# Kernel tuning notes

Hardware: AMD Instinct MI355X
Metric: run time of the kernel (lower is better)

## Reference

```python
import jax, jax.numpy as jnp
import numpy as np

EMB = 256
N_NODES = 100000
N_EDGES = 500000
N_REL = 10
REL_DIM = 64
HID = 128
HEADS = 4
HEAD_DIM = HID // HEADS


def setup_inputs() -> dict:
    key = jax.random.key(0)
    ks = jax.random.split(key, 16)
    s = lambda i, shape: jax.random.normal(ks[i], shape, dtype=jnp.float32) * 0.05
    return {
        "node_embeddings": jax.random.normal(ks[0], (N_NODES, EMB), dtype=jnp.float32),
        "edge_index": jax.random.randint(ks[1], (2, N_EDGES), 0, N_NODES),
        "relation_type": jax.random.randint(ks[2], (N_EDGES,), 0, N_REL),
        "rel_emb": s(3, (N_REL, REL_DIM)),
        "W_edge": s(4, (2 * EMB, HID)), "b_edge": jnp.zeros((HID,), jnp.float32),
        "W_q": s(5, (REL_DIM, HID)), "b_q": jnp.zeros((HID,), jnp.float32),
        "W_k": s(6, (HID, HID)), "b_k": jnp.zeros((HID,), jnp.float32),
        "W_v": s(7, (HID, HID)), "b_v": jnp.zeros((HID,), jnp.float32),
        "W_o1": s(8, (HID, HID)), "b_o1": jnp.zeros((HID,), jnp.float32),
        "W_o2": s(9, (HID, 1)), "b_o2": jnp.zeros((1,), jnp.float32),
    }


def reference(node_embeddings, edge_index, relation_type, rel_emb,
              W_edge, b_edge, W_q, b_q, W_k, b_k, W_v, b_v,
              W_o1, b_o1, W_o2, b_o2):
    # Gather endpoint features: [E, 2*EMB]
    src = node_embeddings[edge_index[0]]
    tgt = node_embeddings[edge_index[1]]
    edge_features = jnp.concatenate([src, tgt], axis=1)
    # Edge MLP (dropout is identity at eval): [E, HID]
    edge_hidden = jax.nn.relu(edge_features @ W_edge + b_edge)
    # Relation embedding lookup: [E, REL_DIM]
    rel = rel_emb[relation_type]
    E = edge_hidden.shape[0]
    Q = (rel @ W_q + b_q).reshape(E, HEADS, HEAD_DIM)
    K = (edge_hidden @ W_k + b_k).reshape(E, HEADS, HEAD_DIM)
    V = (edge_hidden @ W_v + b_v).reshape(E, HEADS, HEAD_DIM)
    scale = jnp.sqrt(jnp.float32(HEAD_DIM))
    scores = jnp.sum(Q * K, axis=-1) / scale          # [E, HEADS]
    attn = jax.nn.softmax(scores, axis=-1)            # softmax over heads
    attended = (attn[..., None] * V).reshape(E, HID)
    output = attended + edge_hidden
    # Output MLP: Linear->ReLU->Linear(1)
    h = jax.nn.relu(output @ W_o1 + b_o1)
    score = (h @ W_o2 + b_o2).squeeze(-1)             # [E]
    return score
```

## Files before the change

kernel.cpp:

```cpp
#include <hip/hip_runtime.h>

#define EMB   256
#define HID   128
#define RELD  64
#define NREL  10
#define TE    64

typedef __attribute__((ext_vector_type(8)))  short bf16x8;
typedef __attribute__((ext_vector_type(16))) float f32x16;

__device__ __forceinline__ float bf16_to_f32(unsigned short u) {
    union { unsigned int i; float f; } v;
    v.i = ((unsigned int)u) << 16;
    return v.f;
}

__device__ __forceinline__ unsigned short f32_to_bf16(float x) {
    union { unsigned int i; float f; } v;
    v.f = x;
    unsigned int b = v.i;
    unsigned int rounded = b + 0x7fffu + ((b >> 16) & 1u);
    return (unsigned short)(rounded >> 16);
}

template <bool F32>
__device__ __forceinline__ float ldx(const void* p, size_t i) {
    if (F32) return ((const float*)p)[i];
    return bf16_to_f32(((const unsigned short*)p)[i]);
}

__device__ __forceinline__ bool detect_f32(const void* nodeEmb) {
    const float* f = (const float*)nodeEmb;
    float x = f[(threadIdx.x & 63) * 997];
    bool sane = isfinite(x) && fabsf(x) < 1.0e6f;
    unsigned long long m = __ballot(sane);
    return __popcll(m) >= 48;
}

template <bool F32>
__device__ void prep_body(int vb, const void* W_edge, const void* W_k,
                          const void* W_v, const void* W_o1, const void* rel_emb,
                          const void* W_q, const void* b_q,
                          unsigned short* WTe, unsigned short* WTk,
                          unsigned short* WTv, unsigned short* WTo1, float* Qtab)
{
    if (vb < 448) {
        int idx = vb * 256 + threadIdx.x;
        if (idx < 65536) {
            int kc = idx >> 12, e = idx & 4095;
            int g = e >> 3, j = e & 7;
            int col = g & 127, kg = g >> 7;
            int k = kc * 32 + kg * 8 + j;
            WTe[idx] = f32_to_bf16(ldx<F32>(W_edge, (size_t)k * HID + col));
        } else if (idx < 65536 + 16384) {
            int i = idx - 65536;
            int kc = i >> 12, e = i & 4095;
            int g = e >> 3, j = e & 7;
            int col = g & 127, kg = (g >> 7) & 3;
            int k = kc * 32 + kg * 8 + j;
            WTk[i] = f32_to_bf16(ldx<F32>(W_k, (size_t)k * HID + col));
        } else if (idx < 65536 + 2 * 16384) {
            int i = idx - 65536 - 16384;
            int kc = i >> 12, e = i & 4095;
            int g = e >> 3, j = e & 7;
            int col = g & 127, kg = (g >> 7) & 3;
            int k = kc * 32 + kg * 8 + j;
            WTv[i] = f32_to_bf16(ldx<F32>(W_v, (size_t)k * HID + col));
        } else {
            int i = idx - 65536 - 2 * 16384;
            int kc = i >> 12, e = i & 4095;
            int g = e >> 3, j = e & 7;
            int col = g & 127, kg = (g >> 7) & 3;
            int k = kc * 32 + kg * 8 + j;
            WTo1[i] = f32_to_bf16(ldx<F32>(W_o1, (size_t)k * HID + col));
        }
    } else {
        const int t = threadIdx.x;
        const int c = t & (HID - 1);
        const int h = t >> 7;
        for (int r = h; r < NREL; r += 2) {
            float acc = 0.f;
            for (int d = 0; d < RELD; ++d)
                acc += ldx<F32>(rel_emb, r * RELD + d) * ldx<F32>(W_q, (size_t)d * HID + c);
            Qtab[r * HID + c] = acc + ldx<F32>(b_q, c);
        }
    }
}

__global__ void prep_kernel(const void* nodeEmb,
                            const void* W_edge, const void* W_k, const void* W_v,
                            const void* W_o1, const void* rel_emb, const void* W_q,
                            const void* b_q,
                            unsigned short* WTe, unsigned short* WTk,
                            unsigned short* WTv, unsigned short* WTo1, float* Qtab,
                            unsigned short* nodeBf16, int convBlocks,
                            unsigned long long nodeElems)
{
    bool f32 = detect_f32(nodeEmb);
    int b = blockIdx.x;
    if (b < convBlocks) {
        if (!f32) return;
        unsigned long long i = (unsigned long long)b * 2048ull + threadIdx.x * 8;
        if (i + 8 <= nodeElems) {
            const float* src = (const float*)nodeEmb + i;
            float4 f0 = *(const float4*)src;
            float4 f1 = *(const float4*)(src + 4);
            union { unsigned short us[8]; uint4 v; } pk;
            pk.us[0] = f32_to_bf16(f0.x); pk.us[1] = f32_to_bf16(f0.y);
            pk.us[2] = f32_to_bf16(f0.z); pk.us[3] = f32_to_bf16(f0.w);
            pk.us[4] = f32_to_bf16(f1.x); pk.us[5] = f32_to_bf16(f1.y);
            pk.us[6] = f32_to_bf16(f1.z); pk.us[7] = f32_to_bf16(f1.w);
            *(uint4*)(nodeBf16 + i) = pk.v;
        }
        return;
    }
    b -= convBlocks;
    if (f32) prep_body<true >(b, W_edge, W_k, W_v, W_o1, rel_emb, W_q, b_q,
                              WTe, WTk, WTv, WTo1, Qtab);
    else     prep_body<false>(b, W_edge, W_k, W_v, W_o1, rel_emb, W_q, b_q,
                              WTe, WTk, WTv, WTo1, Qtab);
}

struct __align__(16) Smem {
    unsigned short sHid[TE][136];
    float sQf[NREL * HID];
    float sBias[5 * HID];
    float sSc[TE][4], sAttn[TE][4];
    float sPart[TE][2];
    int   sSrc[TE], sTgt[TE], sRel[TE];
};

template <bool GBF16>
__device__ __forceinline__ bf16x8 loadA8(const void* row, int off) {
    if (GBF16) {
        return *(const bf16x8*)((const unsigned short*)row + off);
    } else {
        const float* p = (const float*)row + off;
        float4 f0 = *(const float4*)p;
        float4 f1 = *(const float4*)(p + 4);
        union { unsigned short us[8]; bf16x8 v; } pk;
        pk.us[0] = f32_to_bf16(f0.x); pk.us[1] = f32_to_bf16(f0.y);
        pk.us[2] = f32_to_bf16(f0.z); pk.us[3] = f32_to_bf16(f0.w);
        pk.us[4] = f32_to_bf16(f1.x); pk.us[5] = f32_to_bf16(f1.y);
        pk.us[6] = f32_to_bf16(f1.z); pk.us[7] = f32_to_bf16(f1.w);
        return pk.v;
    }
}

template <bool F32, bool GBF16>
__device__ void fused_body(
    Smem& sm,
    const void* gsrc, const int* edgeIdx, const int* relType,
    const unsigned short* WTe, const unsigned short* WTk,
    const unsigned short* WTv, const unsigned short* WTo1,
    const void* b_edge, const void* b_k, const void* b_v,
    const void* b_o1, const void* W_o2, const void* b_o2,
    const float* Qtab, void* outp, int E)
{
    const int t   = threadIdx.x;
    const int l   = t & 63;
    const int w   = t >> 6;
    const int c   = l & 31;
    const int h5  = l >> 5;
    const int rt  = w & 1;
    const int cg2 = w >> 1;
    const int bs  = blockIdx.x * TE;
    const int mye = 32 * rt + c;

    if (t < TE) {
        int e = bs + t;
        if (e >= E) e = E - 1;
        if (e < 0)  e = 0;
        sm.sSrc[t] = edgeIdx[e];
        sm.sTgt[t] = edgeIdx[E + e];
        int r = relType[e];
        if (r < 0) r = 0;
        if (r >= NREL) r = NREL - 1;
        sm.sRel[t] = r;
    }
    for (int i = t; i < 5 * HID; i += 256) {
        int which = i >> 7, j = i & (HID - 1);
        float v = (which == 0) ? ldx<F32>(b_edge, j)
                : (which == 1) ? ldx<F32>(b_k, j)
                : (which == 2) ? ldx<F32>(b_v, j)
                : (which == 3) ? ldx<F32>(b_o1, j)
                               : ldx<F32>(W_o2, j);
        sm.sBias[i] = v;
    }
    for (int i = t; i < NREL * HID; i += 256)
        sm.sQf[i] = Qtab[i];
    __syncthreads();

    const void* rowSrc;
    const void* rowTgt;
    if (GBF16) {
        rowSrc = (const void*)((const unsigned short*)gsrc + (size_t)sm.sSrc[mye] * EMB);
        rowTgt = (const void*)((const unsigned short*)gsrc + (size_t)sm.sTgt[mye] * EMB);
    } else {
        rowSrc = (const void*)((const float*)gsrc + (size_t)sm.sSrc[mye] * EMB);
        rowTgt = (const void*)((const float*)gsrc + (size_t)sm.sTgt[mye] * EMB);
    }

    const int bu = (h5 * 128 + 64 * cg2 + c) * 8;

    f32x16 acc[2];
    acc[0] = (f32x16)(0.0f); acc[1] = (f32x16)(0.0f);
    #pragma unroll
    for (int kc = 0; kc < 16; ++kc) {
        const void* row = (kc < 8) ? rowSrc : rowTgt;
        const int cb = (kc & 7) * 32;
        #pragma unroll
        for (int s = 0; s < 2; ++s) {
            bf16x8 a = loadA8<GBF16>(row, cb + s * 16 + h5 * 8);
            #pragma unroll
            for (int ct = 0; ct < 2; ++ct) {
                bf16x8 b = *(const bf16x8*)(WTe + kc * 4096 + s * 2048 + ct * 256 + bu);
                acc[ct] = __builtin_amdgcn_mfma_f32_32x32x16_bf16(a, b, acc[ct], 0, 0, 0);
            }
        }
    }
    {
        #pragma unroll
        for (int ct = 0; ct < 2; ++ct) {
            int col = 64 * cg2 + 32 * ct + c;
            float bb = sm.sBias[col];
            #pragma unroll
            for (int r = 0; r < 16; ++r) {
                int erow = 32 * rt + (r & 3) + 8 * (r >> 2) + 4 * h5;
                sm.sHid[erow][col] = f32_to_bf16(fmaxf(acc[ct][r] + bb, 0.f));
            }
        }
    }
    __syncthreads();

    f32x16 kacc[2], vacc[2];
    kacc[0] = (f32x16)(0.0f); kacc[1] = (f32x16)(0.0f);
    vacc[0] = (f32x16)(0.0f); vacc[1] = (f32x16)(0.0f);
    #pragma unroll
    for (int kc = 0; kc < 4; ++kc) {
        #pragma unroll
        for (int s = 0; s < 2; ++s) {
            bf16x8 a = *(const bf16x8*)&sm.sHid[mye][kc * 32 + s * 16 + h5 * 8];
            #pragma unroll
            for (int ct = 0; ct < 2; ++ct) {
                bf16x8 bk = *(const bf16x8*)(WTk + kc * 4096 + s * 2048 + ct * 256 + bu);
                bf16x8 bv = *(const bf16x8*)(WTv + kc * 4096 + s * 2048 + ct * 256 + bu);
                kacc[ct] = __builtin_amdgcn_mfma_f32_32x32x16_bf16(a, bk, kacc[ct], 0, 0, 0);
                vacc[ct] = __builtin_amdgcn_mfma_f32_32x32x16_bf16(a, bv, vacc[ct], 0, 0, 0);
            }
        }
    }

    {
        float ps[2][16];
        #pragma unroll
        for (int ct = 0; ct < 2; ++ct) {
            int col = 64 * cg2 + 32 * ct + c;
            float bk = sm.sBias[HID + col];
            #pragma unroll
            for (int r = 0; r < 16; ++r) {
                int erow = 32 * rt + (r & 3) + 8 * (r >> 2) + 4 * h5;
                ps[ct][r] = (kacc[ct][r] + bk) * sm.sQf[sm.sRel[erow] * HID + col];
            }
        }
        #pragma unroll
        for (int m = 1; m < 32; m <<= 1)
            #pragma unroll
            for (int ct = 0; ct < 2; ++ct)
                #pragma unroll
                for (int r = 0; r < 16; ++r)
                    ps[ct][r] += __shfl_xor(ps[ct][r], m, 64);
        if (c == 0) {
            const float inv = 0.17677669529663687f;
            #pragma unroll
            for (int ct = 0; ct < 2; ++ct) {
                int head = 2 * cg2 + ct;
                #pragma unroll
                for (int r = 0; r < 16; ++r) {
                    int erow = 32 * rt + (r & 3) + 8 * (r >> 2) + 4 * h5;
                    sm.sSc[erow][head] = ps[ct][r] * inv;
                }
            }
        }
    }
    __syncthreads();
    if (t < TE) {
        float s0 = sm.sSc[t][0], s1 = sm.sSc[t][1];
        float s2 = sm.sSc[t][2], s3 = sm.sSc[t][3];
        float m = fmaxf(fmaxf(s0, s1), fmaxf(s2, s3));
        float e0 = expf(s0 - m), e1 = expf(s1 - m);
        float e2 = expf(s2 - m), e3 = expf(s3 - m);
        float den = e0 + e1 + e2 + e3;
        sm.sAttn[t][0] = e0 / den; sm.sAttn[t][1] = e1 / den;
        sm.sAttn[t][2] = e2 / den; sm.sAttn[t][3] = e3 / den;
    }
    __syncthreads();

    {
        #pragma unroll
        for (int ct = 0; ct < 2; ++ct) {
            int col  = 64 * cg2 + 32 * ct + c;
            int head = 2 * cg2 + ct;
            float bv = sm.sBias[2 * HID + col];
            #pragma unroll
            for (int r = 0; r < 16; ++r) {
                int erow = 32 * rt + (r & 3) + 8 * (r >> 2) + 4 * h5;
                float at = sm.sAttn[erow][head];
                float hv = bf16_to_f32(sm.sHid[erow][col]);
                sm.sHid[erow][col] = f32_to_bf16(at * (vacc[ct][r] + bv) + hv);
            }
        }
    }
    __syncthreads();

    f32x16 oacc[2];
    oacc[0] = (f32x16)(0.0f); oacc[1] = (f32x16)(0.0f);
    #pragma unroll
    for (int kc = 0; kc < 4; ++kc) {
        #pragma unroll
        for (int s = 0; s < 2; ++s) {
            bf16x8 a = *(const bf16x8*)&sm.sHid[mye][kc * 32 + s * 16 + h5 * 8];
            #pragma unroll
            for (int ct = 0; ct < 2; ++ct) {
                bf16x8 b = *(const bf16x8*)(WTo1 + kc * 4096 + s * 2048 + ct * 256 + bu);
                oacc[ct] = __builtin_amdgcn_mfma_f32_32x32x16_bf16(a, b, oacc[ct], 0, 0, 0);
            }
        }
    }
    {
        float pr[16];
        #pragma unroll
        for (int r = 0; r < 16; ++r) pr[r] = 0.f;
        #pragma unroll
        for (int ct = 0; ct < 2; ++ct) {
            int col = 64 * cg2 + 32 * ct + c;
            float bo = sm.sBias[3 * HID + col];
            float wo = sm.sBias[4 * HID + col];
            #pragma unroll
            for (int r = 0; r < 16; ++r)
                pr[r] += fmaxf(oacc[ct][r] + bo, 0.f) * wo;
        }
        #pragma unroll
        for (int m = 1; m < 32; m <<= 1)
            #pragma unroll
            for (int r = 0; r < 16; ++r)
                pr[r] += __shfl_xor(pr[r], m, 64);
        if (c == 0) {
            #pragma unroll
            for (int r = 0; r < 16; ++r) {
                int erow = 32 * rt + (r & 3) + 8 * (r >> 2) + 4 * h5;
                sm.sPart[erow][cg2] = pr[r];
            }
        }
    }
    __syncthreads();
    if (t < TE) {
        int ge = bs + t;
        if (ge < E) {
            float val = sm.sPart[t][0] + sm.sPart[t][1] + ldx<F32>(b_o2, 0);
            if (F32) ((float*)outp)[ge] = val;
            else     ((unsigned short*)outp)[ge] = f32_to_bf16(val);
        }
    }
}

__global__ __launch_bounds__(256, 4) void RelationAttentionMLPHead_10539849744626_kernel(
    const void* nodeEmb, const unsigned short* nodeBf16, int useConv,
    const int* edgeIdx, const int* relType,
    const unsigned short* WTe, const unsigned short* WTk,
    const unsigned short* WTv, const unsigned short* WTo1,
    const void* b_edge, const void* b_k, const void* b_v,
    const void* b_o1, const void* W_o2, const void* b_o2,
    const float* Qtab, void* outp, int E)
{
    __shared__ Smem sm;
    if (detect_f32(nodeEmb)) {
        if (useConv)
            fused_body<true, true >(sm, nodeBf16, edgeIdx, relType, WTe, WTk, WTv, WTo1,
                                    b_edge, b_k, b_v, b_o1, W_o2, b_o2, Qtab, outp, E);
        else
            fused_body<true, false>(sm, nodeEmb, edgeIdx, relType, WTe, WTk, WTv, WTo1,
                                    b_edge, b_k, b_v, b_o1, W_o2, b_o2, Qtab, outp, E);
    } else {
        fused_body<false, true>(sm, nodeEmb, edgeIdx, relType, WTe, WTk, WTv, WTo1,
                                b_edge, b_k, b_v, b_o1, W_o2, b_o2, Qtab, outp, E);
    }
}

extern "C" void kernel_launch(void* const* d_in, const int* in_sizes, int n_in,
                              void* d_out, int out_size, void* d_ws, size_t ws_size,
                              hipStream_t stream) {
    (void)n_in;

    const void* nodeEmb = d_in[0];
    const int*  edgeIdx = (const int*)d_in[1];
    const int*  relType = (const int*)d_in[2];
    const void* rel_emb = d_in[3];
    const void* W_edge  = d_in[4];
    const void* b_edge  = d_in[5];
    const void* W_q     = d_in[6];
    const void* b_q     = d_in[7];
    const void* W_k     = d_in[8];
    const void* b_k     = d_in[9];
    const void* W_v     = d_in[10];
    const void* b_v     = d_in[11];
    const void* W_o1    = d_in[12];
    const void* b_o1    = d_in[13];
    const void* W_o2    = d_in[14];
    const void* b_o2    = d_in[15];

    int E = out_size;
    if (E <= 0) E = in_sizes ? in_sizes[2] : 0;
    if (E <= 0) E = 500000;

    unsigned long long nodeElems =
        (in_sizes && in_sizes[0] > 0) ? (unsigned long long)in_sizes[0] : 25600000ull;

    char* ws = (char*)d_ws;
    float*          Qtab     = (float*)ws;
    unsigned short* WTe      = (unsigned short*)(ws + 8192);
    unsigned short* WTk      = (unsigned short*)(ws + 139264);
    unsigned short* WTv      = (unsigned short*)(ws + 172032);
    unsigned short* WTo1     = (unsigned short*)(ws + 204800);
    unsigned short* nodeBf16 = (unsigned short*)(ws + 237568);

    size_t need = 237568ull + nodeElems * 2ull;
    int useConv = (ws_size >= need) ? 1 : 0;
    int convBlocks = useConv ? (int)((nodeElems + 2047ull) / 2048ull) : 0;

    prep_kernel<<<convBlocks + 449, 256, 0, stream>>>(
        nodeEmb, W_edge, W_k, W_v, W_o1, rel_emb, W_q, b_q,
        WTe, WTk, WTv, WTo1, Qtab, nodeBf16, convBlocks, nodeElems);

    int grid = (E + TE - 1) / TE;
    if (grid < 1) grid = 1;

    RelationAttentionMLPHead_10539849744626_kernel<<<grid, 256, 0, stream>>>(
        nodeEmb, nodeBf16, useConv, edgeIdx, relType, WTe, WTk, WTv, WTo1,
        b_edge, b_k, b_v, b_o1, W_o2, b_o2, Qtab, d_out, E);
}
```

Measured before the change: 452.9 us.

## Double tile to 128 edges, software-pipeline edge GEMM loads, swizzle hidden smem layout

Doubles the edge tile to 128 edges with 512-thread blocks and remaps waves to row/column groups. The edge-MLP loop now prefetches A rows three k-steps ahead and B weights two steps ahead in registers. K, V and O1 weights are preloaded into registers ahead of their GEMMs, and the hidden buffer in LDS uses a k-group-major layout to avoid bank conflicts. Barriers are replaced by an explicit lgkmcnt wait plus s_barrier. The added register pressure may hurt occupancy under the 512,4 launch bounds.

After: 555.2 us. 1.23x slower.

```diff
diff --git a/kernel.cpp b/kernel.cpp
--- a/kernel.cpp
+++ b/kernel.cpp
@@ -4,7 +4,7 @@
 #define HID   128
 #define RELD  64
 #define NREL  10
-#define TE    64
+#define TE    128
 
 typedef __attribute__((ext_vector_type(8)))  short bf16x8;
 typedef __attribute__((ext_vector_type(16))) float f32x16;
@@ -35,6 +35,12 @@
     bool sane = isfinite(x) && fabsf(x) < 1.0e6f;
     unsigned long long m = __ballot(sane);
     return __popcll(m) >= 48;
+}
+
+__device__ __forceinline__ void barrier_lgkm() {
+    asm volatile("s_waitcnt lgkmcnt(0)" ::: "memory");
+    __builtin_amdgcn_s_barrier();
+    __builtin_amdgcn_sched_barrier(0);
 }
 
 template <bool F32>
@@ -122,13 +128,18 @@
 }
 
 struct __align__(16) Smem {
-    unsigned short sHid[TE][136];
+    unsigned short sHid[16 * 128 * 8];
     float sQf[NREL * HID];
     float sBias[5 * HID];
-    float sSc[TE][4], sAttn[TE][4];
+    float sSc[TE][4];
+    float sAttn[TE][4];
     float sPart[TE][2];
     int   sSrc[TE], sTgt[TE], sRel[TE];
 };
+
+__device__ __forceinline__ int shid_idx(int row, int k) {
+    return (((k >> 3) * 128 + row) << 3) + (k & 7);
+}
 
 template <bool GBF16>
 __device__ __forceinline__ bf16x8 loadA8(const void* row, int off) {
@@ -162,10 +173,10 @@
     const int w   = t >> 6;
     const int c   = l & 31;
     const int h5  = l >> 5;
-    const int rt  = w & 1;
-    const int cg2 = w >> 1;
+    const int rt  = w >> 1;
+    const int cg2 = w & 1;
     const int bs  = blockIdx.x * TE;
-    const int mye = 32 * rt + c;
+    const int aRow = 32 * rt + c;
 
     if (t < TE) {
         int e = bs + t;
@@ -178,7 +189,7 @@
         if (r >= NREL) r = NREL - 1;
         sm.sRel[t] = r;
     }
-    for (int i = t; i < 5 * HID; i += 256) {
+    for (int i = t; i < 5 * HID; i += 512) {
         int which = i >> 7, j = i & (HID - 1);
         float v = (which == 0) ? ldx<F32>(b_edge, j)
                 : (which == 1) ? ldx<F32>(b_k, j)
@@ -187,38 +198,75 @@
                                : ldx<F32>(W_o2, j);
         sm.sBias[i] = v;
     }
-    for (int i = t; i < NREL * HID; i += 256)
+    for (int i = t; i < NREL * HID; i += 512)
         sm.sQf[i] = Qtab[i];
-    __syncthreads();
+    barrier_lgkm();
 
     const void* rowSrc;
     const void* rowTgt;
     if (GBF16) {
-        rowSrc = (const void*)((const unsigned short*)gsrc + (size_t)sm.sSrc[mye] * EMB);
-        rowTgt = (const void*)((const unsigned short*)gsrc + (size_t)sm.sTgt[mye] * EMB);
+        rowSrc = (const void*)((const unsigned short*)gsrc + (size_t)sm.sSrc[aRow] * EMB);
+        rowTgt = (const void*)((const unsigned short*)gsrc + (size_t)sm.sTgt[aRow] * EMB);
     } else {
-        rowSrc = (const void*)((const float*)gsrc + (size_t)sm.sSrc[mye] * EMB);
-        rowTgt = (const void*)((const float*)gsrc + (size_t)sm.sTgt[mye] * EMB);
+        rowSrc = (const void*)((const float*)gsrc + (size_t)sm.sSrc[aRow] * EMB);
+        rowTgt = (const void*)((const float*)gsrc + (size_t)sm.sTgt[aRow] * EMB);
     }
 
     const int bu = (h5 * 128 + 64 * cg2 + c) * 8;
+
+    #define LOAD_A(kc, s) \
+        loadA8<GBF16>(((kc) < 8) ? rowSrc : rowTgt, ((kc) & 7) * 32 + (s) * 16 + h5 * 8)
+    #define LDB(WT, kc, s, ct) \
+        (*(const bf16x8*)((WT) + bu + (kc) * 4096 + (s) * 2048 + (ct) * 256))
 
     f32x16 acc[2];
     acc[0] = (f32x16)(0.0f); acc[1] = (f32x16)(0.0f);
+    {
+        bf16x8 aR[4][2];
+        bf16x8 bR[2][2][2];
+        #pragma unroll
+        for (int p = 0; p < 3; ++p) {
+            aR[p][0] = LOAD_A(p, 0);
+            aR[p][1] = LOAD_A(p, 1);
+        }
+        #pragma unroll
+        for (int p = 0; p < 2; ++p)
+            #pragma unroll
+            for (int s = 0; s < 2; ++s)
+                #pragma unroll
+                for (int ct = 0; ct < 2; ++ct)
+                    bR[p][s][ct] = LDB(WTe, p, s, ct);
+        #pragma unroll
+        for (int kc = 0; kc < 16; ++kc) {
+            if (kc < 13) {
+                aR[(kc + 3) & 3][0] = LOAD_A(kc + 3, 0);
+                aR[(kc + 3) & 3][1] = LOAD_A(kc + 3, 1);
+            }
+            #pragma unroll
+            for (int s = 0; s < 2; ++s)
+                #pragma unroll
+                for (int ct = 0; ct < 2; ++ct)
+                    acc[ct] = __builtin_amdgcn_mfma_f32_32x32x16_bf16(
+                        aR[kc & 3][s], bR[kc & 1][s][ct], acc[ct], 0, 0, 0);
+            if (kc < 14) {
+                #pragma unroll
+                for (int s = 0; s < 2; ++s)
+                    #pragma unroll
+                    for (int ct = 0; ct < 2; ++ct)
+                        bR[kc & 1][s][ct] = LDB(WTe, kc + 2, s, ct);
+            }
+        }
+    }
+
+    bf16x8 bK[4][2][2];
     #pragma unroll
-    for (int kc = 0; kc < 16; ++kc) {
-        const void* row = (kc < 8) ? rowSrc : rowTgt;
-        const int cb = (kc & 7) * 32;
-        #pragma unroll
-        for (int s = 0; s < 2; ++s) {
-            bf16x8 a = loadA8<GBF16>(row, cb + s * 16 + h5 * 8);
-            #pragma unroll
-            for (int ct = 0; ct < 2; ++ct) {
-                bf16x8 b = *(const bf16x8*)(WTe + kc * 4096 + s * 2048 + ct * 256 + bu);
-                acc[ct] = __builtin_amdgcn_mfma_f32_32x32x16_bf16(a, b, acc[ct], 0, 0, 0);
-            }
-        }
-    }
+    for (int kc = 0; kc < 4; ++kc)
+        #pragma unroll
+        for (int s = 0; s < 2; ++s)
+            #pragma unroll
+            for (int ct = 0; ct < 2; ++ct)
+                bK[kc][s][ct] = LDB(WTk, kc, s, ct);
+
     {
         #pragma unroll
         for (int ct = 0; ct < 2; ++ct) {
@@ -227,29 +275,34 @@
             #pragma unroll
             for (int r = 0; r < 16; ++r) {
                 int erow = 32 * rt + (r & 3) + 8 * (r >> 2) + 4 * h5;
-                sm.sHid[erow][col] = f32_to_bf16(fmaxf(acc[ct][r] + bb, 0.f));
-            }
-        }
-    }
-    __syncthreads();
-
-    f32x16 kacc[2], vacc[2];
+                sm.sHid[shid_idx(erow, col)] = f32_to_bf16(fmaxf(acc[ct][r] + bb, 0.f));
+            }
+        }
+    }
+    barrier_lgkm();
+
+    f32x16 kacc[2];
     kacc[0] = (f32x16)(0.0f); kacc[1] = (f32x16)(0.0f);
-    vacc[0] = (f32x16)(0.0f); vacc[1] = (f32x16)(0.0f);
     #pragma unroll
-    for (int kc = 0; kc < 4; ++kc) {
+    for (int kc = 0; kc < 4; ++kc)
         #pragma unroll
         for (int s = 0; s < 2; ++s) {
-            bf16x8 a = *(const bf16x8*)&sm.sHid[mye][kc * 32 + s * 16 + h5 * 8];
-            #pragma unroll
-            for (int ct = 0; ct < 2; ++ct) {
-                bf16x8 bk = *(const bf16x8*)(WTk + kc * 4096 + s * 2048 + ct * 256 + bu);
-                bf16x8 bv = *(const bf16x8*)(WTv + kc * 4096 + s * 2048 + ct * 256 + bu);
-                kacc[ct] = __builtin_amdgcn_mfma_f32_32x32x16_bf16(a, bk, kacc[ct], 0, 0, 0);
-                vacc[ct] = __builtin_amdgcn_mfma_f32_32x32x16_bf16(a, bv, vacc[ct], 0, 0, 0);
-            }
-        }
-    }
+            bf16x8 a = *(const bf16x8*)((const char*)sm.sHid +
+                         (((kc * 4 + s * 2 + h5) * 128 + aRow) << 4));
+            #pragma unroll
+            for (int ct = 0; ct < 2; ++ct)
+                kacc[ct] = __builtin_amdgcn_mfma_f32_32x32x16_bf16(
+                    a, bK[kc][s][ct], kacc[ct], 0, 0, 0);
+        }
+
+    bf16x8 bV[4][2][2];
+    #pragma unroll
+    for (int kc = 0; kc < 4; ++kc)
+        #pragma unroll
+        for (int s = 0; s < 2; ++s)
+            #pragma unroll
+            for (int ct = 0; ct < 2; ++ct)
+                bV[kc][s][ct] = LDB(WTv, kc, s, ct);
 
     {
         float ps[2][16];
@@ -283,7 +336,7 @@
             }
         }
     }
-    __syncthreads();
+    barrier_lgkm();
     if (t < TE) {
         float s0 = sm.sSc[t][0], s1 = sm.sSc[t][1];
         float s2 = sm.sSc[t][2], s3 = sm.sSc[t][3];
@@ -294,7 +347,32 @@
         sm.sAttn[t][0] = e0 / den; sm.sAttn[t][1] = e1 / den;
         sm.sAttn[t][2] = e2 / den; sm.sAttn[t][3] = e3 / den;
     }
-    __syncthreads();
+    barrier_lgkm();
+
+    f32x16 vacc[2];
+    vacc[0] = (f32x16)(0.0f); vacc[1] = (f32x16)(0.0f);
+    #pragma unroll
+    for (int kc = 0; kc < 4; ++kc)
+        #pragma unroll
+        for (int s = 0; s < 2; ++s) {
+            bf16x8 a = *(const bf16x8*)((const char*)sm.sHid +
+                         (((kc * 4 + s * 2 + h5) * 128 + aRow) << 4));
+            #pragma unroll
+            for (int ct = 0; ct < 2; ++ct)
+                vacc[ct] = __builtin_amdgcn_mfma_f32_32x32x16_bf16(
+                    a, bV[kc][s][ct], vacc[ct], 0, 0, 0);
+        }
+
+    bf16x8 bO[4][2][2];
+    #pragma unroll
+    for (int kc = 0; kc < 4; ++kc)
+        #pragma unroll
+        for (int s = 0; s < 2; ++s)
+            #pragma unroll
+            for (int ct = 0; ct < 2; ++ct)
+                bO[kc][s][ct] = LDB(WTo1, kc, s, ct);
+
+    barrier_lgkm();
 
     {
         #pragma unroll
@@ -306,27 +384,27 @@
             for (int r = 0; r < 16; ++r) {
                 int erow = 32 * rt + (r & 3) + 8 * (r >> 2) + 4 * h5;
                 float at = sm.sAttn[erow][head];
-                float hv = bf16_to_f32(sm.sHid[erow][col]);
-                sm.sHid[erow][col] = f32_to_bf16(at * (vacc[ct][r] + bv) + hv);
-            }
-        }
-    }
-    __syncthreads();
+                int   si = shid_idx(erow, col);
+                float hv = bf16_to_f32(sm.sHid[si]);
+                sm.sHid[si] = f32_to_bf16(at * (vacc[ct][r] + bv) + hv);
+            }
+        }
+    }
+    barrier_lgkm();
 
     f32x16 oacc[2];
     oacc[0] = (f32x16)(0.0f); oacc[1] = (f32x16)(0.0f);
     #pragma unroll
-    for (int kc = 0; kc < 4; ++kc) {
+    for (int kc = 0; kc < 4; ++kc)
         #pragma unroll
         for (int s = 0; s < 2; ++s) {
-            bf16x8 a = *(const bf16x8*)&sm.sHid[mye][kc * 32 + s * 16 + h5 * 8];
-            #pragma unroll
-            for (int ct = 0; ct < 2; ++ct) {
-                bf16x8 b = *(const bf16x8*)(WTo1 + kc * 4096 + s * 2048 + ct * 256 + bu);
-                oacc[ct] = __builtin_amdgcn_mfma_f32_32x32x16_bf16(a, b, oacc[ct], 0, 0, 0);
-            }
-        }
-    }
+            bf16x8 a = *(const bf16x8*)((const char*)sm.sHid +
+                         (((kc * 4 + s * 2 + h5) * 128 + aRow) << 4));
+            #pragma unroll
+            for (int ct = 0; ct < 2; ++ct)
+                oacc[ct] = __builtin_amdgcn_mfma_f32_32x32x16_bf16(
+                    a, bO[kc][s][ct], oacc[ct], 0, 0, 0);
+        }
     {
         float pr[16];
         #pragma unroll
@@ -353,7 +431,7 @@
             }
         }
     }
-    __syncthreads();
+    barrier_lgkm();
     if (t < TE) {
         int ge = bs + t;
         if (ge < E) {
@@ -362,9 +440,12 @@
             else     ((unsigned short*)outp)[ge] = f32_to_bf16(val);
         }
     }
-}
-
-__global__ __launch_bounds__(256, 4) void RelationAttentionMLPHead_10539849744626_kernel(
+
+    #undef LOAD_A
+    #undef LDB
+}
+
+__global__ __launch_bounds__(512, 4) void RelationAttentionMLPHead_10539849744626_kernel(
     const void* nodeEmb, const unsigned short* nodeBf16, int useConv,
     const int* edgeIdx, const int* relType,
     const unsigned short* WTe, const unsigned short* WTk,
@@ -435,7 +516,7 @@
     int grid = (E + TE - 1) / TE;
     if (grid < 1) grid = 1;
 
-    RelationAttentionMLPHead_10539849744626_kernel<<<grid, 256, 0, stream>>>(
+    RelationAttentionMLPHead_10539849744626_kernel<<<grid, 512, 0, stream>>>(
         nodeEmb, nodeBf16, useConv, edgeIdx, relType, WTe, WTk, WTv, WTo1,
         b_edge, b_k, b_v, b_o1, W_o2, b_o2, Qtab, d_out, E);
 }
```
